# Optimization experiments

Hardware: AMD Instinct MI355X
Metric: run time of the kernel (lower is better)

The kernel has to match this reference:

```python
import jax, jax.numpy as jnp
import numpy as np

N_EMBD = 1024
N_HEAD = 16
HEAD_DIM = N_EMBD // N_HEAD


def setup_inputs() -> dict:
    key = jax.random.key(0)
    ks = jax.random.split(key, 6)
    B, T, C = 4, 2048, N_EMBD
    scale = 1.0 / np.sqrt(C)
    x = jax.random.normal(ks[0], (B, T, C), dtype=jnp.float32)
    Wq = jax.random.normal(ks[1], (C, C), dtype=jnp.float32) * scale
    Wk = jax.random.normal(ks[2], (C, C), dtype=jnp.float32) * scale
    Wv = jax.random.normal(ks[3], (C, C), dtype=jnp.float32) * scale
    Wo = jax.random.normal(ks[4], (C, C), dtype=jnp.float32) * scale
    bo = jax.random.normal(ks[5], (C,), dtype=jnp.float32) * 0.01
    return {"x": x, "Wq": Wq, "Wk": Wk, "Wv": Wv, "Wo": Wo, "bo": bo}


def reference(x, Wq, Wk, Wv, Wo, bo):
    B, T, C = x.shape
    H, D = N_HEAD, HEAD_DIM
    # projections (torch Linear: x @ W.T); reshape to [B, H, T, D]
    q = (x @ Wq.T).reshape(B, T, H, D).transpose(0, 2, 1, 3)
    k = (x @ Wk.T).reshape(B, T, H, D).transpose(0, 2, 1, 3)
    v = (x @ Wv.T).reshape(B, T, H, D).transpose(0, 2, 1, 3)
    scores = jnp.einsum("bhqd,bhkd->bhqk", q, k) / np.sqrt(D)
    causal = jnp.tril(jnp.ones((T, T), dtype=bool))  # True = keep
    scores = jnp.where(causal, scores, -jnp.inf)
    attn = jax.nn.softmax(scores, axis=-1)
    # dropout in eval mode = identity
    out = jnp.einsum("bhqk,bhkd->bhqd", attn, v)
    out = out.transpose(0, 2, 1, 3).reshape(B, T, C)
    return out @ Wo.T + bo
```

## Files before the change

kernel.cpp:

```cpp
#include <hip/hip_runtime.h>

typedef __attribute__((ext_vector_type(4))) float floatx4;
typedef __attribute__((ext_vector_type(8))) __bf16 bf16x8;
typedef __attribute__((ext_vector_type(8))) unsigned short ushort8;
typedef __attribute__((ext_vector_type(4))) unsigned short ushort4v;

#define MFMA16(a, b, c) __builtin_amdgcn_mfma_f32_16x16x32_bf16((a), (b), (c), 0, 0, 0)

static __device__ __forceinline__ unsigned short f2bu(float f) {
  unsigned int u = __builtin_bit_cast(unsigned int, f);
  unsigned int r = (u + 0x7fffu + ((u >> 16) & 1u)) >> 16;
  return (unsigned short)r;
}

static __device__ __forceinline__ unsigned int cvtpk(float lo, float hi) {
  unsigned int r;
  asm("v_cvt_pk_bf16_f32 %0, %1, %2" : "=v"(r) : "v"(lo), "v"(hi));
  return r;
}

static __device__ __forceinline__ void gload_lds16(const void* g, void* l) {
  __builtin_amdgcn_global_load_lds((const __attribute__((address_space(1))) void*)g,
                                   (__attribute__((address_space(3))) void*)l, 16, 0, 0);
}

__global__ void cast_f32_bf16(const float* __restrict__ src, unsigned short* __restrict__ dst, int n4) {
  int i = blockIdx.x * blockDim.x + threadIdx.x;
  if (i >= n4) return;
  float4 v = reinterpret_cast<const float4*>(src)[i];
  ushort4v o;
  o.x = f2bu(v.x); o.y = f2bu(v.y); o.z = f2bu(v.z); o.w = f2bu(v.w);
  reinterpret_cast<ushort4v*>(dst)[i] = o;
}

static __device__ __forceinline__ void gemm_core(const unsigned short* __restrict__ Ag,
                                                 const unsigned short* __restrict__ Wg,
                                                 int tm0, int tn0,
                                                 unsigned short* As, unsigned short* Bs,
                                                 floatx4 acc[4][4]) {
  const int tid = threadIdx.x;
  const int w = tid >> 6, l = tid & 63;
  const int lg = l >> 4, lq = l & 15;
  const int wr = w >> 1, wc = w & 1;

  const int srow = w * 32 + (l >> 2);
  const int scol = (l & 3) * 8;
  const unsigned short* ga = Ag + (size_t)(tm0 + srow) * 1024 + scol;
  const unsigned short* gb = Wg + (size_t)(tn0 + srow) * 1024 + scol;
  unsigned short* la0 = As + (w * 32) * 32;
  unsigned short* la1 = la0 + 16 * 32;
  unsigned short* lb0 = Bs + (w * 32) * 32;
  unsigned short* lb1 = lb0 + 16 * 32;

  for (int kt = 0; kt < 32; ++kt) {
    gload_lds16(ga + kt * 32, la0);
    gload_lds16(ga + 16 * 1024 + kt * 32, la1);
    gload_lds16(gb + kt * 32, lb0);
    gload_lds16(gb + 16 * 1024 + kt * 32, lb1);
    __syncthreads();
    bf16x8 ar[4], br[4];
#pragma unroll
    for (int i = 0; i < 4; ++i) {
      ar[i] = *(const bf16x8*)(As + (wr * 64 + i * 16 + lq) * 32 + lg * 8);
      br[i] = *(const bf16x8*)(Bs + (wc * 64 + i * 16 + lq) * 32 + lg * 8);
    }
#pragma unroll
    for (int i = 0; i < 4; ++i)
#pragma unroll
      for (int j = 0; j < 4; ++j)
        acc[i][j] = MFMA16(ar[i], br[j], acc[i][j]);
    __syncthreads();
  }
}

__global__ __launch_bounds__(256) void gemm_qkv(const unsigned short* __restrict__ xb,
                                                const unsigned short* __restrict__ Wqb,
                                                const unsigned short* __restrict__ Wkb,
                                                const unsigned short* __restrict__ Wvb,
                                                unsigned short* __restrict__ Qb,
                                                unsigned short* __restrict__ Kb,
                                                unsigned short* __restrict__ Vtb) {
  __shared__ unsigned short As[128 * 32];
  __shared__ unsigned short Bs[128 * 32];
  const int tid = threadIdx.x;
  const int w = tid >> 6, l = tid & 63;
  const int lg = l >> 4, lq = l & 15;
  const int wr = w >> 1, wc = w & 1;
  const int tm0 = blockIdx.x * 128;
  const int tn0 = blockIdx.y * 128;
  const int z = blockIdx.z;
  const unsigned short* W = (z == 0) ? Wqb : (z == 1) ? Wkb : Wvb;

  floatx4 acc[4][4];
#pragma unroll
  for (int i = 0; i < 4; ++i)
#pragma unroll
    for (int j = 0; j < 4; ++j) acc[i][j] = (floatx4){0.f, 0.f, 0.f, 0.f};

  gemm_core(xb, W, tm0, tn0, As, Bs, acc);

  const int b = tm0 >> 11;
  const int t0 = tm0 & 2047;

  if (z == 2) {
#pragma unroll
    for (int mi = 0; mi < 4; ++mi)
#pragma unroll
      for (int ni = 0; ni < 4; ++ni) {
        int t = t0 + wr * 64 + mi * 16 + lg * 4;
        int n = tn0 + wc * 64 + ni * 16 + lq;
        int h = n >> 6, d = n & 63;
        ushort4v o;
        o.x = f2bu(acc[mi][ni][0]);
        o.y = f2bu(acc[mi][ni][1]);
        o.z = f2bu(acc[mi][ni][2]);
        o.w = f2bu(acc[mi][ni][3]);
        *(ushort4v*)(Vtb + ((size_t)(b * 16 + h) * 64 + d) * 2048 + t) = o;
      }
  } else {
    float sc = (z == 0) ? 0.125f * 1.44269504f : 1.0f;
    unsigned short* dst = (z == 0) ? Qb : Kb;
#pragma unroll
    for (int mi = 0; mi < 4; ++mi)
#pragma unroll
      for (int ni = 0; ni < 4; ++ni) {
        int n = tn0 + wc * 64 + ni * 16 + lq;
        int h = n >> 6, d = n & 63;
#pragma unroll
        for (int r = 0; r < 4; ++r) {
          int t = t0 + wr * 64 + mi * 16 + lg * 4 + r;
          dst[((size_t)(b * 16 + h) * 2048 + t) * 64 + d] = f2bu(acc[mi][ni][r] * sc);
        }
      }
  }
}

__global__ __launch_bounds__(256) void attn_fwd(const unsigned short* __restrict__ Qb,
                                                const unsigned short* __restrict__ Kb,
                                                const unsigned short* __restrict__ Vtb,
                                                unsigned short* __restrict__ attb) {
  constexpr int T = 2048;
  __shared__ char Ls[32768];
  const int bh = blockIdx.x;
  const int pr = blockIdx.y;
  const int tid = threadIdx.x;
  const int w = tid >> 6, l = tid & 63;
  const int lg = l >> 4, lq = l & 15;

  const char* Kgc = (const char*)(Kb + (size_t)bh * T * 64);
  const char* Vgc = (const char*)(Vtb + (size_t)bh * 64 * T);
  const unsigned short* Qp = Qb + (size_t)bh * T * 64;

  const int srow = w * 8 + (l >> 3);
  const int scolx = ((l & 7) << 4) ^ ((l >> 3) << 4);
  const int koff0 = srow * 128 + scolx;
  const int koff1 = koff0 + 32 * 128;
  const int voff0 = srow * 4096 + scolx;
  const int voff1 = voff0 + 32 * 4096;
  char* Ks = (char*)Ls;
  char* Vs = (char*)Ls + 16384;
  const int kswz = (lq & 7) << 4;

  const int b = bh >> 4, h = bh & 15;

#define STAGE(bi, kb_)                                          \
  do {                                                          \
    const char* kg_ = Kgc + (size_t)(kb_) * 128;                \
    const char* vg_ = Vgc + (size_t)(kb_) * 2;                  \
    gload_lds16(kg_ + koff0, Ks + (bi) * 8192 + w * 1024);      \
    gload_lds16(kg_ + koff1, Ks + (bi) * 8192 + (w + 4) * 1024);\
    gload_lds16(vg_ + voff0, Vs + (bi) * 8192 + w * 1024);      \
    gload_lds16(vg_ + voff1, Vs + (bi) * 8192 + (w + 4) * 1024);\
  } while (0)

  for (int pi = 0; pi < 2; ++pi) {
    const int qt = pi ? (15 - pr) : pr;
    const int q0 = qt * 128 + w * 32;

    bf16x8 qf[2][2];
#pragma unroll
    for (int qh = 0; qh < 2; ++qh)
#pragma unroll
      for (int dh = 0; dh < 2; ++dh)
        qf[qh][dh] = *(const bf16x8*)(Qp + (size_t)(q0 + qh * 16 + lq) * 64 + dh * 32 + lg * 8);

    floatx4 acc[2][4];
#pragma unroll
    for (int qh = 0; qh < 2; ++qh)
#pragma unroll
      for (int dc = 0; dc < 4; ++dc) acc[qh][dc] = (floatx4){0.f, 0.f, 0.f, 0.f};
    float m_run[2] = {-1e30f, -1e30f};
    float l_run[2] = {0.f, 0.f};

    const int nt = 2 * qt + 2;
    int buf = 0;
    STAGE(0, 0);
    __syncthreads();

    for (int t = 0; t < nt; ++t) {
      if (t + 1 < nt) STAGE(buf ^ 1, (t + 1) * 64);
      if (t * 64 <= q0 + 31) {
        const char* Kl = Ks + buf * 8192;
        const char* Vl = Vs + buf * 8192;
        const int kb = t * 64;

        floatx4 s[2][4];
#pragma unroll
        for (int kc = 0; kc < 4; ++kc) {
          const int rowb = (kc * 16 + lq) * 128;
          bf16x8 kf0 = *(const bf16x8*)(Kl + rowb + ((lg * 16) ^ kswz));
          bf16x8 kf1 = *(const bf16x8*)(Kl + rowb + ((64 + lg * 16) ^ kswz));
#pragma unroll
          for (int qh = 0; qh < 2; ++qh) {
            floatx4 tt = (floatx4){0.f, 0.f, 0.f, 0.f};
            tt = MFMA16(kf0, qf[qh][0], tt);
            tt = MFMA16(kf1, qf[qh][1], tt);
            s[qh][kc] = tt;
          }
        }

        if (kb + 63 > q0) {
#pragma unroll
          for (int qh = 0; qh < 2; ++qh) {
            const int qrow = q0 + qh * 16 + lq;
#pragma unroll
            for (int kc = 0; kc < 4; ++kc)
#pragma unroll
              for (int r = 0; r < 4; ++r)
                if (kb + kc * 16 + lg * 4 + r > qrow) s[qh][kc][r] = -1e30f;
          }
        }

        bf16x8 pa[2][2];
#pragma unroll
        for (int qh = 0; qh < 2; ++qh) {
          float mt = -1e30f;
#pragma unroll
          for (int kc = 0; kc < 4; ++kc)
#pragma unroll
            for (int r = 0; r < 4; ++r) mt = fmaxf(mt, s[qh][kc][r]);
          mt = fmaxf(mt, __shfl_xor(mt, 16, 64));
          mt = fmaxf(mt, __shfl_xor(mt, 32, 64));
          float m_new = fmaxf(m_run[qh], mt);
          float corr = exp2f(m_run[qh] - m_new);
          float p[4][4];
          float rs = 0.f;
#pragma unroll
          for (int kc = 0; kc < 4; ++kc)
#pragma unroll
            for (int r = 0; r < 4; ++r) {
              float e = exp2f(s[qh][kc][r] - m_new);
              p[kc][r] = e;
              rs += e;
            }
          rs += __shfl_xor(rs, 16, 64);
          rs += __shfl_xor(rs, 32, 64);
          l_run[qh] = l_run[qh] * corr + rs;
          m_run[qh] = m_new;
#pragma unroll
          for (int dc = 0; dc < 4; ++dc) acc[qh][dc] *= corr;
          int4 u0, u1;
          u0.x = cvtpk(p[0][0], p[0][1]); u0.y = cvtpk(p[0][2], p[0][3]);
          u0.z = cvtpk(p[1][0], p[1][1]); u0.w = cvtpk(p[1][2], p[1][3]);
          u1.x = cvtpk(p[2][0], p[2][1]); u1.y = cvtpk(p[2][2], p[2][3]);
          u1.z = cvtpk(p[3][0], p[3][1]); u1.w = cvtpk(p[3][2], p[3][3]);
          pa[qh][0] = __builtin_bit_cast(bf16x8, u0);
          pa[qh][1] = __builtin_bit_cast(bf16x8, u1);
        }

#pragma unroll
        for (int dc = 0; dc < 4; ++dc) {
          const int rowb = (dc * 16 + lq) * 128;
#pragma unroll
          for (int kk = 0; kk < 2; ++kk) {
            ushort4v v0 = *(const ushort4v*)(Vl + rowb + ((kk * 64 + lg * 8) ^ kswz));
            ushort4v v1 = *(const ushort4v*)(Vl + rowb + ((kk * 64 + lg * 8 + 32) ^ kswz));
            ushort8 vv = __builtin_shufflevector(v0, v1, 0, 1, 2, 3, 4, 5, 6, 7);
            bf16x8 va = __builtin_bit_cast(bf16x8, vv);
#pragma unroll
            for (int qh = 0; qh < 2; ++qh)
              acc[qh][dc] = MFMA16(va, pa[qh][kk], acc[qh][dc]);
          }
        }
      }
      __syncthreads();
      buf ^= 1;
    }

#pragma unroll
    for (int qh = 0; qh < 2; ++qh) {
      float inv = 1.f / l_run[qh];
      unsigned short* orow = attb + (size_t)(b * 2048 + q0 + qh * 16 + lq) * 1024 + h * 64;
#pragma unroll
      for (int dc = 0; dc < 4; ++dc) {
        ushort4v o;
        o.x = f2bu(acc[qh][dc][0] * inv);
        o.y = f2bu(acc[qh][dc][1] * inv);
        o.z = f2bu(acc[qh][dc][2] * inv);
        o.w = f2bu(acc[qh][dc][3] * inv);
        *(ushort4v*)(orow + 16 * dc + lg * 4) = o;
      }
    }
  }
#undef STAGE
}

__global__ __launch_bounds__(256) void gemm_out(const unsigned short* __restrict__ attb,
                                                const unsigned short* __restrict__ Wob,
                                                const float* __restrict__ bo,
                                                float* __restrict__ out) {
  __shared__ unsigned short As[128 * 32];
  __shared__ unsigned short Bs[128 * 32];
  const int tid = threadIdx.x;
  const int w = tid >> 6, l = tid & 63;
  const int lg = l >> 4, lq = l & 15;
  const int wr = w >> 1, wc = w & 1;
  const int tm0 = blockIdx.x * 128;
  const int tn0 = blockIdx.y * 128;

  floatx4 acc[4][4];
#pragma unroll
  for (int i = 0; i < 4; ++i)
#pragma unroll
    for (int j = 0; j < 4; ++j) acc[i][j] = (floatx4){0.f, 0.f, 0.f, 0.f};

  gemm_core(attb, Wob, tm0, tn0, As, Bs, acc);

#pragma unroll
  for (int mi = 0; mi < 4; ++mi)
#pragma unroll
    for (int ni = 0; ni < 4; ++ni) {
      int row = tm0 + wr * 64 + mi * 16 + lg * 4;
      int col = tn0 + wc * 64 + ni * 16 + lq;
      float bias = bo[col];
#pragma unroll
      for (int r = 0; r < 4; ++r)
        out[(size_t)(row + r) * 1024 + col] = acc[mi][ni][r] + bias;
    }
}

extern "C" void kernel_launch(void* const* d_in, const int* in_sizes, int n_in,
                              void* d_out, int out_size, void* d_ws, size_t ws_size,
                              hipStream_t stream) {
  const float* x  = (const float*)d_in[0];
  const float* Wq = (const float*)d_in[1];
  const float* Wk = (const float*)d_in[2];
  const float* Wv = (const float*)d_in[3];
  const float* Wo = (const float*)d_in[4];
  const float* bo = (const float*)d_in[5];
  float* out = (float*)d_out;

  unsigned short* ws = (unsigned short*)d_ws;
  unsigned short* xb  = ws;
  unsigned short* Wqb = ws + 8388608;
  unsigned short* Wkb = ws + 9437184;
  unsigned short* Wvb = ws + 10485760;
  unsigned short* Wob = ws + 11534336;
  unsigned short* Qb  = ws + 12582912;
  unsigned short* Kb  = ws + 20971520;
  unsigned short* Vtb = ws + 29360128;
  unsigned short* attb= ws + 37748736;

  cast_f32_bf16<<<8192, 256, 0, stream>>>(x, xb, 2097152);
  cast_f32_bf16<<<1024, 256, 0, stream>>>(Wq, Wqb, 262144);
  cast_f32_bf16<<<1024, 256, 0, stream>>>(Wk, Wkb, 262144);
  cast_f32_bf16<<<1024, 256, 0, stream>>>(Wv, Wvb, 262144);
  cast_f32_bf16<<<1024, 256, 0, stream>>>(Wo, Wob, 262144);

  gemm_qkv<<<dim3(64, 8, 3), 256, 0, stream>>>(xb, Wqb, Wkb, Wvb, Qb, Kb, Vtb);
  attn_fwd<<<dim3(64, 8), 256, 0, stream>>>(Qb, Kb, Vtb, attb);
  gemm_out<<<dim3(64, 8), 256, 0, stream>>>(attb, Wob, bo, out);
}
```

Measured before the change: 290.6 us.

## Shrink attention query tile to 64 rows and add lazy softmax rescaling

The attention kernel now processes 64-query tiles, with 16 rows per wave, and launches twice as many blocks. This removes the skipped and partially masked iterations that 128-row tiles wasted on the causal diagonal. The running max is only updated when the new max exceeds the old one by a threshold (11 in log2 units), so the accumulator rescale is skipped most of the time. Row sums are computed with an MFMA against a ones vector instead of shuffles, and exp2 uses the raw v_exp_f32 instruction. In exchange, each block reuses each staged K/V tile for fewer queries, and the unnormalized values can grow larger before a rescale happens.

```diff
diff --git a/kernel.cpp b/kernel.cpp
--- a/kernel.cpp
+++ b/kernel.cpp
@@ -16,6 +16,12 @@
 static __device__ __forceinline__ unsigned int cvtpk(float lo, float hi) {
   unsigned int r;
   asm("v_cvt_pk_bf16_f32 %0, %1, %2" : "=v"(r) : "v"(lo), "v"(hi));
+  return r;
+}
+
+static __device__ __forceinline__ float fexp2(float x) {
+  float r;
+  asm("v_exp_f32 %0, %1" : "=v"(r) : "v"(x));
   return r;
 }
 
@@ -151,155 +157,130 @@
   const char* Vgc = (const char*)(Vtb + (size_t)bh * 64 * T);
   const unsigned short* Qp = Qb + (size_t)bh * T * 64;
 
-  const int srow = w * 8 + (l >> 3);
-  const int scolx = ((l & 7) << 4) ^ ((l >> 3) << 4);
-  const int koff0 = srow * 128 + scolx;
-  const int koff1 = koff0 + 32 * 128;
-  const int voff0 = srow * 4096 + scolx;
-  const int voff1 = voff0 + 32 * 4096;
+  const int scolx = ((tid & 7) << 4) ^ (((tid >> 3) & 7) << 4);
+  const int koff = ((tid >> 3) << 7) + scolx;
+  const int voff = ((tid >> 3) << 12) + scolx;
   char* Ks = (char*)Ls;
   char* Vs = (char*)Ls + 16384;
   const int kswz = (lq & 7) << 4;
-
+  const int wofs = w * 1024;
   const int b = bh >> 4, h = bh & 15;
 
-#define STAGE(bi, kb_)                                          \
-  do {                                                          \
-    const char* kg_ = Kgc + (size_t)(kb_) * 128;                \
-    const char* vg_ = Vgc + (size_t)(kb_) * 2;                  \
-    gload_lds16(kg_ + koff0, Ks + (bi) * 8192 + w * 1024);      \
-    gload_lds16(kg_ + koff1, Ks + (bi) * 8192 + (w + 4) * 1024);\
-    gload_lds16(vg_ + voff0, Vs + (bi) * 8192 + w * 1024);      \
-    gload_lds16(vg_ + voff1, Vs + (bi) * 8192 + (w + 4) * 1024);\
+  const ushort8 onesu = {0x3F80, 0x3F80, 0x3F80, 0x3F80, 0x3F80, 0x3F80, 0x3F80, 0x3F80};
+  const bf16x8 onesf = __builtin_bit_cast(bf16x8, onesu);
+
+#define STAGE(bi, kb_)                                               \
+  do {                                                               \
+    const char* kg_ = Kgc + (size_t)(kb_) * 128 + koff;              \
+    const char* vg_ = Vgc + (size_t)(kb_) * 2 + voff;                \
+    gload_lds16(kg_,          Ks + (bi) * 8192 + wofs);              \
+    gload_lds16(kg_ + 4096,   Ks + (bi) * 8192 + 4096 + wofs);       \
+    gload_lds16(vg_,          Vs + (bi) * 8192 + wofs);              \
+    gload_lds16(vg_ + 131072, Vs + (bi) * 8192 + 4096 + wofs);       \
   } while (0)
 
   for (int pi = 0; pi < 2; ++pi) {
-    const int qt = pi ? (15 - pr) : pr;
-    const int q0 = qt * 128 + w * 32;
-
-    bf16x8 qf[2][2];
-#pragma unroll
-    for (int qh = 0; qh < 2; ++qh)
-#pragma unroll
-      for (int dh = 0; dh < 2; ++dh)
-        qf[qh][dh] = *(const bf16x8*)(Qp + (size_t)(q0 + qh * 16 + lq) * 64 + dh * 32 + lg * 8);
-
-    floatx4 acc[2][4];
-#pragma unroll
-    for (int qh = 0; qh < 2; ++qh)
-#pragma unroll
-      for (int dc = 0; dc < 4; ++dc) acc[qh][dc] = (floatx4){0.f, 0.f, 0.f, 0.f};
-    float m_run[2] = {-1e30f, -1e30f};
-    float l_run[2] = {0.f, 0.f};
-
-    const int nt = 2 * qt + 2;
+    const int qt = pi ? (31 - pr) : pr;
+    const int q0 = qt * 64 + w * 16;
+    const int qrow = q0 + lq;
+
+    bf16x8 qf0 = *(const bf16x8*)(Qp + (size_t)qrow * 64 + lg * 8);
+    bf16x8 qf1 = *(const bf16x8*)(Qp + (size_t)qrow * 64 + 32 + lg * 8);
+
+    floatx4 acc[4];
+#pragma unroll
+    for (int dc = 0; dc < 4; ++dc) acc[dc] = (floatx4){0.f, 0.f, 0.f, 0.f};
+    floatx4 rsum = (floatx4){0.f, 0.f, 0.f, 0.f};
+    float m_run = -1e30f;
+
     int buf = 0;
     STAGE(0, 0);
     __syncthreads();
 
-    for (int t = 0; t < nt; ++t) {
-      if (t + 1 < nt) STAGE(buf ^ 1, (t + 1) * 64);
-      if (t * 64 <= q0 + 31) {
-        const char* Kl = Ks + buf * 8192;
-        const char* Vl = Vs + buf * 8192;
-        const int kb = t * 64;
-
-        floatx4 s[2][4];
-#pragma unroll
-        for (int kc = 0; kc < 4; ++kc) {
-          const int rowb = (kc * 16 + lq) * 128;
-          bf16x8 kf0 = *(const bf16x8*)(Kl + rowb + ((lg * 16) ^ kswz));
-          bf16x8 kf1 = *(const bf16x8*)(Kl + rowb + ((64 + lg * 16) ^ kswz));
-#pragma unroll
-          for (int qh = 0; qh < 2; ++qh) {
-            floatx4 tt = (floatx4){0.f, 0.f, 0.f, 0.f};
-            tt = MFMA16(kf0, qf[qh][0], tt);
-            tt = MFMA16(kf1, qf[qh][1], tt);
-            s[qh][kc] = tt;
-          }
-        }
-
-        if (kb + 63 > q0) {
-#pragma unroll
-          for (int qh = 0; qh < 2; ++qh) {
-            const int qrow = q0 + qh * 16 + lq;
-#pragma unroll
-            for (int kc = 0; kc < 4; ++kc)
-#pragma unroll
-              for (int r = 0; r < 4; ++r)
-                if (kb + kc * 16 + lg * 4 + r > qrow) s[qh][kc][r] = -1e30f;
-          }
-        }
-
-        bf16x8 pa[2][2];
-#pragma unroll
-        for (int qh = 0; qh < 2; ++qh) {
-          float mt = -1e30f;
-#pragma unroll
-          for (int kc = 0; kc < 4; ++kc)
-#pragma unroll
-            for (int r = 0; r < 4; ++r) mt = fmaxf(mt, s[qh][kc][r]);
-          mt = fmaxf(mt, __shfl_xor(mt, 16, 64));
-          mt = fmaxf(mt, __shfl_xor(mt, 32, 64));
-          float m_new = fmaxf(m_run[qh], mt);
-          float corr = exp2f(m_run[qh] - m_new);
-          float p[4][4];
-          float rs = 0.f;
-#pragma unroll
-          for (int kc = 0; kc < 4; ++kc)
-#pragma unroll
-            for (int r = 0; r < 4; ++r) {
-              float e = exp2f(s[qh][kc][r] - m_new);
-              p[kc][r] = e;
-              rs += e;
-            }
-          rs += __shfl_xor(rs, 16, 64);
-          rs += __shfl_xor(rs, 32, 64);
-          l_run[qh] = l_run[qh] * corr + rs;
-          m_run[qh] = m_new;
-#pragma unroll
-          for (int dc = 0; dc < 4; ++dc) acc[qh][dc] *= corr;
-          int4 u0, u1;
-          u0.x = cvtpk(p[0][0], p[0][1]); u0.y = cvtpk(p[0][2], p[0][3]);
-          u0.z = cvtpk(p[1][0], p[1][1]); u0.w = cvtpk(p[1][2], p[1][3]);
-          u1.x = cvtpk(p[2][0], p[2][1]); u1.y = cvtpk(p[2][2], p[2][3]);
-          u1.z = cvtpk(p[3][0], p[3][1]); u1.w = cvtpk(p[3][2], p[3][3]);
-          pa[qh][0] = __builtin_bit_cast(bf16x8, u0);
-          pa[qh][1] = __builtin_bit_cast(bf16x8, u1);
-        }
-
-#pragma unroll
-        for (int dc = 0; dc < 4; ++dc) {
-          const int rowb = (dc * 16 + lq) * 128;
-#pragma unroll
-          for (int kk = 0; kk < 2; ++kk) {
-            ushort4v v0 = *(const ushort4v*)(Vl + rowb + ((kk * 64 + lg * 8) ^ kswz));
-            ushort4v v1 = *(const ushort4v*)(Vl + rowb + ((kk * 64 + lg * 8 + 32) ^ kswz));
-            ushort8 vv = __builtin_shufflevector(v0, v1, 0, 1, 2, 3, 4, 5, 6, 7);
-            bf16x8 va = __builtin_bit_cast(bf16x8, vv);
-#pragma unroll
-            for (int qh = 0; qh < 2; ++qh)
-              acc[qh][dc] = MFMA16(va, pa[qh][kk], acc[qh][dc]);
-          }
+    for (int t = 0; t <= qt; ++t) {
+      if (t < qt) STAGE(buf ^ 1, (t + 1) * 64);
+      const char* Kl = Ks + buf * 8192;
+      const char* Vl = Vs + buf * 8192;
+      const int kb = t * 64;
+
+      floatx4 s[4];
+#pragma unroll
+      for (int kc = 0; kc < 4; ++kc) {
+        const int rowb = (kc * 16 + lq) * 128;
+        bf16x8 kf0 = *(const bf16x8*)(Kl + rowb + ((lg * 16) ^ kswz));
+        bf16x8 kf1 = *(const bf16x8*)(Kl + rowb + ((64 + lg * 16) ^ kswz));
+        floatx4 tt = (floatx4){0.f, 0.f, 0.f, 0.f};
+        tt = MFMA16(kf0, qf0, tt);
+        tt = MFMA16(kf1, qf1, tt);
+        s[kc] = tt;
+      }
+
+      if (t == qt) {
+#pragma unroll
+        for (int kc = 0; kc < 4; ++kc)
+#pragma unroll
+          for (int r = 0; r < 4; ++r)
+            if (kb + kc * 16 + lg * 4 + r > qrow) s[kc][r] = -1e30f;
+      }
+
+      float m0 = fmaxf(fmaxf(s[0][0], s[0][1]), fmaxf(s[0][2], s[0][3]));
+      float m1 = fmaxf(fmaxf(s[1][0], s[1][1]), fmaxf(s[1][2], s[1][3]));
+      float m2 = fmaxf(fmaxf(s[2][0], s[2][1]), fmaxf(s[2][2], s[2][3]));
+      float m3 = fmaxf(fmaxf(s[3][0], s[3][1]), fmaxf(s[3][2], s[3][3]));
+      float mt = fmaxf(fmaxf(m0, m1), fmaxf(m2, m3));
+      mt = fmaxf(mt, __shfl_xor(mt, 16, 64));
+      mt = fmaxf(mt, __shfl_xor(mt, 32, 64));
+      if (__any(mt > m_run + 11.f)) {
+        float mn = fmaxf(m_run, mt);
+        float corr = fexp2(m_run - mn);
+#pragma unroll
+        for (int dc = 0; dc < 4; ++dc) acc[dc] *= corr;
+        rsum *= corr;
+        m_run = mn;
+      }
+      float p[4][4];
+#pragma unroll
+      for (int kc = 0; kc < 4; ++kc)
+#pragma unroll
+        for (int r = 0; r < 4; ++r) p[kc][r] = fexp2(s[kc][r] - m_run);
+
+      int4 u0, u1;
+      u0.x = cvtpk(p[0][0], p[0][1]); u0.y = cvtpk(p[0][2], p[0][3]);
+      u0.z = cvtpk(p[1][0], p[1][1]); u0.w = cvtpk(p[1][2], p[1][3]);
+      u1.x = cvtpk(p[2][0], p[2][1]); u1.y = cvtpk(p[2][2], p[2][3]);
+      u1.z = cvtpk(p[3][0], p[3][1]); u1.w = cvtpk(p[3][2], p[3][3]);
+      bf16x8 pa0 = __builtin_bit_cast(bf16x8, u0);
+      bf16x8 pa1 = __builtin_bit_cast(bf16x8, u1);
+
+      rsum = MFMA16(onesf, pa0, rsum);
+      rsum = MFMA16(onesf, pa1, rsum);
+
+#pragma unroll
+      for (int dc = 0; dc < 4; ++dc) {
+        const int rowb = (dc * 16 + lq) * 128;
+#pragma unroll
+        for (int kk = 0; kk < 2; ++kk) {
+          ushort4v v0 = *(const ushort4v*)(Vl + rowb + ((kk * 64 + lg * 8) ^ kswz));
+          ushort4v v1 = *(const ushort4v*)(Vl + rowb + ((kk * 64 + lg * 8 + 32) ^ kswz));
+          ushort8 vv = __builtin_shufflevector(v0, v1, 0, 1, 2, 3, 4, 5, 6, 7);
+          bf16x8 va = __builtin_bit_cast(bf16x8, vv);
+          acc[dc] = MFMA16(va, kk ? pa1 : pa0, acc[dc]);
         }
       }
       __syncthreads();
       buf ^= 1;
     }
 
-#pragma unroll
-    for (int qh = 0; qh < 2; ++qh) {
-      float inv = 1.f / l_run[qh];
-      unsigned short* orow = attb + (size_t)(b * 2048 + q0 + qh * 16 + lq) * 1024 + h * 64;
-#pragma unroll
-      for (int dc = 0; dc < 4; ++dc) {
-        ushort4v o;
-        o.x = f2bu(acc[qh][dc][0] * inv);
-        o.y = f2bu(acc[qh][dc][1] * inv);
-        o.z = f2bu(acc[qh][dc][2] * inv);
-        o.w = f2bu(acc[qh][dc][3] * inv);
-        *(ushort4v*)(orow + 16 * dc + lg * 4) = o;
-      }
+    float inv = 1.f / rsum[0];
+    unsigned short* orow = attb + (size_t)(b * 2048 + qrow) * 1024 + h * 64;
+#pragma unroll
+    for (int dc = 0; dc < 4; ++dc) {
+      ushort4v o;
+      o.x = f2bu(acc[dc][0] * inv);
+      o.y = f2bu(acc[dc][1] * inv);
+      o.z = f2bu(acc[dc][2] * inv);
+      o.w = f2bu(acc[dc][3] * inv);
+      *(ushort4v*)(orow + 16 * dc + lg * 4) = o;
     }
   }
 #undef STAGE
@@ -368,6 +349,6 @@
   cast_f32_bf16<<<1024, 256, 0, stream>>>(Wo, Wob, 262144);
 
   gemm_qkv<<<dim3(64, 8, 3), 256, 0, stream>>>(xb, Wqb, Wkb, Wvb, Qb, Kb, Vtb);
-  attn_fwd<<<dim3(64, 8), 256, 0, stream>>>(Qb, Kb, Vtb, attb);
+  attn_fwd<<<dim3(64, 16), 256, 0, stream>>>(Qb, Kb, Vtb, attb);
   gemm_out<<<dim3(64, 8), 256, 0, stream>>>(attb, Wob, bo, out);
 }
```

Result: faster. 266.8 us (-8.2%).
